# Optimization experiments

Measured on AMD Instinct MI355X. Metric: run time of the kernel, lower is better.

The kernel has to match this reference:

```python
import jax, jax.numpy as jnp
import numpy as np

NUM_CELLS, NUM_CLASSES = 25, 17
B = 65536
MULT = 16            # multiplier
OC = 64              # out_channels = out_features // 25
OUT_FEATURES = 1600
SLOPE = 0.01         # F.leaky_relu default negative_slope


def lrelu(x):
    return jax.nn.leaky_relu(x, SLOPE)


def setup_inputs() -> dict:
    key = jax.random.key(0)
    ks = jax.random.split(key, 9)
    s = 0.05
    return {
        "x": jax.random.randint(ks[0], (B, NUM_CELLS), 0, NUM_CLASSES, dtype=jnp.int64)
             if jax.config.jax_enable_x64 else
             jax.random.randint(ks[0], (B, NUM_CELLS), 0, NUM_CLASSES).astype(jnp.int32),
        # depthwise_full: Conv1d(17, 425, 25, groups=17) -> per-group [17, 25, 25]
        "W_df": jax.random.normal(ks[1], (NUM_CLASSES, NUM_CELLS, NUM_CELLS), jnp.float32) * s,
        "b_df": jnp.zeros((NUM_CLASSES * NUM_CELLS,), jnp.float32),
        # pointwise_full: Conv1d(425, 320, 1)
        "W_pf": jax.random.normal(ks[2], (OC * 5, NUM_CLASSES * NUM_CELLS), jnp.float32) * s,
        "b_pf": jax.random.normal(ks[3], (OC * 5,), jnp.float32) * s,
        # depthwise_hori: Conv2d(17, 272, (1,5), groups=17) -> [17, 16, 5]
        "W_dh": jax.random.normal(ks[4], (NUM_CLASSES, MULT, 5), jnp.float32) * s,
        "b_dh": jnp.zeros((NUM_CLASSES * MULT,), jnp.float32),
        "W_ph": jax.random.normal(ks[5], (OC, NUM_CLASSES * MULT), jnp.float32) * s,
        "b_ph": jax.random.normal(ks[5], (OC,), jnp.float32) * s,
        # depthwise_vert: Conv2d(17, 272, (5,1), groups=17) -> [17, 16, 5]
        "W_dv": jax.random.normal(ks[6], (NUM_CLASSES, MULT, 5), jnp.float32) * s,
        "b_dv": jnp.zeros((NUM_CLASSES * MULT,), jnp.float32),
        "W_pv": jax.random.normal(ks[7], (OC, NUM_CLASSES * MULT), jnp.float32) * s,
        "b_pv": jax.random.normal(ks[7], (OC,), jnp.float32) * s,
        # conv_out: Conv1d(64, 1600, 15)
        "W_out": jax.random.normal(ks[8], (OUT_FEATURES, OC, 15), jnp.float32) * s,
        "b_out": jnp.zeros((OUT_FEATURES,), jnp.float32),
    }


def reference(x, W_df, b_df, W_pf, b_pf, W_dh, b_dh, W_ph, b_ph,
              W_dv, b_dv, W_pv, b_pv, W_out, b_out):
    b = x.shape[0]
    oh = jax.nn.one_hot(x, NUM_CLASSES, dtype=jnp.float32)       # [B,25,17]
    xc = jnp.transpose(oh, (0, 2, 1))                            # [B,17,25]

    # full branch: depthwise conv1d k=25 over length-25 -> length 1
    full = jnp.einsum('bcl,cml->bcm', xc, W_df).reshape(b, -1) + b_df   # [B,425]
    full = lrelu(full)
    full = lrelu(full @ W_pf.T + b_pf)                           # [B,320]

    board = xc.reshape(b, NUM_CLASSES, 5, 5)                     # [B,17,5,5]

    # horizontal: depthwise (1,5) conv -> [B,272,5] (over rows)
    hori = jnp.einsum('bcrj,cmj->bcmr', board, W_dh).reshape(b, -1, 5) + b_dh[None, :, None]
    hori = lrelu(hori)
    hori = lrelu(jnp.einsum('bkr,ok->bor', hori, W_ph) + b_ph[None, :, None])  # [B,64,5]

    # vertical: depthwise (5,1) conv -> [B,272,5] (over cols)
    vert = jnp.einsum('bcrj,cmr->bcmj', board, W_dv).reshape(b, -1, 5) + b_dv[None, :, None]
    vert = lrelu(vert)
    vert = lrelu(jnp.einsum('bkj,ok->boj', vert, W_pv) + b_pv[None, :, None])  # [B,64,5]

    cat = jnp.concatenate([full.reshape(b, OC, 5), hori, vert], axis=2)        # [B,64,15]
    out = lrelu(jnp.einsum('bcl,ocl->bo', cat, W_out) + b_out)                 # [B,1600]
    return out
```

## Files before the change

### kernel.cpp

```cpp
#include <hip/hip_runtime.h>


typedef __bf16 bf16;
typedef bf16  bf16x8 __attribute__((ext_vector_type(8)));
typedef float f32x4  __attribute__((ext_vector_type(4)));

__device__ __forceinline__ float lrelu(float v) { return v > 0.f ? v : 0.01f * v; }

__device__ __forceinline__ void gl2lds16(const void* g, void* l) {
  __builtin_amdgcn_global_load_lds(
      (__attribute__((address_space(1))) void*)const_cast<void*>(g),
      (__attribute__((address_space(3))) void*)l, 16, 0, 0);
}

__device__ __forceinline__ void xcd_remap(int& mt, int& nt) {
  const int nxt    = gridDim.x;
  const int nwg    = gridDim.x * gridDim.y;
  const int linear = blockIdx.y * gridDim.x + blockIdx.x;
  const int xcd = linear & 7, pos = linear >> 3;
  const int q = nwg >> 3, r = nwg & 7;
  const int logical = (xcd < r ? xcd * (q + 1) : r * (q + 1) + (xcd - r) * q) + pos;
  mt = logical / nxt;
  nt = logical - mt * nxt;
}

__device__ void compute_U(float* __restrict__ U,
                          const float* __restrict__ Wd, const float* __restrict__ bd,
                          const float* __restrict__ Wp, const float* __restrict__ bp,
                          int c, int mask, int o) {
  float val;
  if (mask == 0) {
    if (c == 0) {
      float s = bp[o];
      for (int cc = 0; cc < 17; cc++)
        for (int m = 0; m < 16; m++)
          s += Wp[o * 272 + cc * 16 + m] * lrelu(bd[cc * 16 + m]);
      val = s;
    } else {
      val = 0.f;
    }
  } else {
    float s = 0.f;
    #pragma unroll
    for (int m = 0; m < 16; m++) {
      float z = bd[c * 16 + m];
      #pragma unroll
      for (int j = 0; j < 5; j++)
        if ((mask >> j) & 1) z += Wd[c * 80 + m * 5 + j];
      s += Wp[o * 272 + c * 16 + m] * (lrelu(z) - lrelu(bd[c * 16 + m]));
    }
    val = s;
  }
  U[(c * 32 + mask) * 64 + o] = val;
}

__global__ __launch_bounds__(256) void prep_kernel(
    const float* __restrict__ W_pf,
    const float* __restrict__ W_dh, const float* __restrict__ b_dh,
    const float* __restrict__ W_ph, const float* __restrict__ b_ph,
    const float* __restrict__ W_dv, const float* __restrict__ b_dv,
    const float* __restrict__ W_pv, const float* __restrict__ b_pv,
    const float* __restrict__ W_out,
    bf16* __restrict__ WbOT, bf16* __restrict__ WbPF,
    float* __restrict__ Uh, float* __restrict__ Uv) {
  int id = blockIdx.x * 256 + threadIdx.x;

  if (id < 1664 * 960) {
    int n = id / 960, k = id % 960;
    float v = 0.f;
    if (n < 1600) {
      int src;
      if (k < 320)      src = n * 960 + (k / 5) * 15 + (k % 5);
      else if (k < 640) { int kk = k - 320; src = n * 960 + (kk & 63) * 15 + 5  + (kk >> 6); }
      else              { int kk = k - 640; src = n * 960 + (kk & 63) * 15 + 10 + (kk >> 6); }
      v = W_out[src];
    }
    WbOT[id] = (bf16)v;
    return;
  }
  id -= 1664 * 960;

  if (id < 384 * 448) {
    int n = id / 448, k = id % 448;
    float v = (n < 320 && k < 425) ? W_pf[n * 425 + k] : 0.f;
    WbPF[id] = (bf16)v;
    return;
  }
  id -= 384 * 448;

  if (id < 17 * 32 * 64) {
    int o = id & 63, rest = id >> 6;
    compute_U(Uh, W_dh, b_dh, W_ph, b_ph, rest >> 5, rest & 31, o);
    return;
  }
  id -= 17 * 32 * 64;

  if (id < 17 * 32 * 64) {
    int o = id & 63, rest = id >> 6;
    compute_U(Uv, W_dv, b_dv, W_pv, b_pv, rest >> 5, rest & 31, o);
  }
}

#define AF_PAD 456

__global__ __launch_bounds__(256) void build_afull(
    const int* __restrict__ x, const float* __restrict__ W_df,
    const float* __restrict__ b_df, bf16* __restrict__ a_full) {
  __shared__ int  xs[64 * 25];
  __shared__ bf16 as[64 * AF_PAD];
  const int b0 = blockIdx.x * 64;
  for (int i = threadIdx.x; i < 64 * 25; i += 256) xs[i] = x[(long)b0 * 25 + i];
  __syncthreads();

  const int wave = threadIdx.x >> 6, lane = threadIdx.x & 63;
  for (int role = wave; role < 18; role += 4) {
    if (role < 17) {
      const int c = role;
      float acc[25];
      #pragma unroll
      for (int m = 0; m < 25; m++) acc[m] = 0.f;
      #pragma unroll
      for (int l = 0; l < 25; l++) {
        int xl = xs[lane * 25 + l];
        if (xl == c) {
          #pragma unroll
          for (int m = 0; m < 25; m++) acc[m] += W_df[c * 625 + m * 25 + l];
        }
      }
      #pragma unroll
      for (int m = 0; m < 25; m++)
        as[lane * AF_PAD + c * 25 + m] = (bf16)lrelu(acc[m] + b_df[c * 25 + m]);
    } else {
      for (int k = 425; k < 448; k++) as[lane * AF_PAD + k] = (bf16)0.f;
    }
  }
  __syncthreads();

  int4* dst = (int4*)(a_full + (long)b0 * 448);
  for (int i = threadIdx.x; i < 3584; i += 256) {
    int row = i / 56, off = i % 56;
    dst[i] = *(const int4*)((const char*)as + row * (AF_PAD * 2) + off * 16);
  }
}

__device__ __forceinline__ float group5(const float* __restrict__ U, int lane,
                                        int c0, int c1, int c2, int c3, int c4) {
  float acc = U[lane];
  {
    int m = 1 | ((int)(c1 == c0) << 1) | ((int)(c2 == c0) << 2) |
                ((int)(c3 == c0) << 3) | ((int)(c4 == c0) << 4);
    acc += U[(c0 * 32 + m) * 64 + lane];
  }
  if (c1 != c0) {
    int m = 2 | ((int)(c2 == c1) << 2) | ((int)(c3 == c1) << 3) | ((int)(c4 == c1) << 4);
    acc += U[(c1 * 32 + m) * 64 + lane];
  }
  if (c2 != c0 && c2 != c1) {
    int m = 4 | ((int)(c3 == c2) << 3) | ((int)(c4 == c2) << 4);
    acc += U[(c2 * 32 + m) * 64 + lane];
  }
  if (c3 != c0 && c3 != c1 && c3 != c2) {
    int m = 8 | ((int)(c4 == c3) << 4);
    acc += U[(c3 * 32 + m) * 64 + lane];
  }
  if (c4 != c0 && c4 != c1 && c4 != c2 && c4 != c3) {
    acc += U[(c4 * 32 + 16) * 64 + lane];
  }
  return lrelu(acc);
}

__global__ __launch_bounds__(256) void hv_kernel(
    const int* __restrict__ x, const float* __restrict__ Uh,
    const float* __restrict__ Uv, bf16* __restrict__ cat) {
  const int wave = threadIdx.x >> 6, lane = threadIdx.x & 63;
  const long b = (long)blockIdx.x * 4 + wave;
  const int* xb = x + b * 25;
  int xv[25];
  #pragma unroll
  for (int i = 0; i < 25; i++) xv[i] = xb[i];
  bf16* catb = cat + b * 960;
  #pragma unroll
  for (int r = 0; r < 5; r++) {
    float v = group5(Uh, lane, xv[5*r], xv[5*r+1], xv[5*r+2], xv[5*r+3], xv[5*r+4]);
    catb[320 + r * 64 + lane] = (bf16)v;
  }
  #pragma unroll
  for (int j = 0; j < 5; j++) {
    float v = group5(Uv, lane, xv[j], xv[5+j], xv[10+j], xv[15+j], xv[20+j]);
    catb[640 + j * 64 + lane] = (bf16)v;
  }
}

template <int KT, int MODE>
__global__ __launch_bounds__(256, 2) void gemm_bt(
    const bf16* __restrict__ A, const bf16* __restrict__ Bt,
    const float* __restrict__ bias, bf16* __restrict__ outb,
    float* __restrict__ outf, const int Nwrite, const int ldOut) {
  static_assert(KT % 32 == 0, "KT must be multiple of 32");
  __shared__ bf16 As[128 * 32];
  __shared__ bf16 Bs[128 * 32];

  const int tid = threadIdx.x;
  const int wave = tid >> 6, lane = tid & 63;
  int mt, nt;
  xcd_remap(mt, nt);

  const int  lrow = lane >> 2, lcol = lane & 3;
  const bf16* ag0 = A  + ((long)mt * 128 + wave * 32 + lrow) * KT + lcol * 8;
  const bf16* bg0 = Bt + ((long)nt * 128 + wave * 32 + lrow) * KT + lcol * 8;
  bf16* al = &As[(wave * 32 + lrow) * 32 + lcol * 8];
  bf16* bl = &Bs[(wave * 32 + lrow) * 32 + lcol * 8];

  const int wm = (wave & 1) * 64;
  const int wn = (wave >> 1) * 64;
  const int fr = lane & 15;
  const int fq = lane >> 4;

  f32x4 acc[4][4];
  #pragma unroll
  for (int i = 0; i < 4; i++)
    #pragma unroll
    for (int j = 0; j < 4; j++) acc[i][j] = f32x4{0.f, 0.f, 0.f, 0.f};

  for (int kt = 0; kt < KT / 32; kt++) {
    const int ko = kt * 32;
    gl2lds16(ag0 + ko, al);
    gl2lds16(ag0 + ko + (long)16 * KT, al + 16 * 32);
    gl2lds16(bg0 + ko, bl);
    gl2lds16(bg0 + ko + (long)16 * KT, bl + 16 * 32);
    __syncthreads();

    bf16x8 af[4], bfv[4];
    #pragma unroll
    for (int i = 0; i < 4; i++)
      af[i] = *(const bf16x8*)&As[(wm + i * 16 + fr) * 32 + fq * 8];
    #pragma unroll
    for (int j = 0; j < 4; j++)
      bfv[j] = *(const bf16x8*)&Bs[(wn + j * 16 + fr) * 32 + fq * 8];
    #pragma unroll
    for (int i = 0; i < 4; i++)
      #pragma unroll
      for (int j = 0; j < 4; j++)
        acc[i][j] = __builtin_amdgcn_mfma_f32_16x16x32_bf16(af[i], bfv[j], acc[i][j], 0, 0, 0);
    __syncthreads();
  }

  #pragma unroll
  for (int j = 0; j < 4; j++) {
    const int n = nt * 128 + wn + j * 16 + fr;
    const bool ok = n < Nwrite;
    const float bv = ok ? bias[n] : 0.f;
    #pragma unroll
    for (int i = 0; i < 4; i++) {
      const long row0 = (long)mt * 128 + wm + i * 16 + fq * 4;
      #pragma unroll
      for (int r = 0; r < 4; r++) {
        float v = lrelu(acc[i][j][r] + bv);
        if (ok) {
          if (MODE == 0) outb[(row0 + r) * (long)ldOut + n] = (bf16)v;
          else           outf[(row0 + r) * (long)ldOut + n] = v;
        }
      }
    }
  }
}

extern "C" void kernel_launch(void* const* d_in, const int* in_sizes, int n_in,
                              void* d_out, int out_size, void* d_ws, size_t ws_size,
                              hipStream_t stream) {
  const int*   x     = (const int*)d_in[0];
  const float* W_df  = (const float*)d_in[1];
  const float* b_df  = (const float*)d_in[2];
  const float* W_pf  = (const float*)d_in[3];
  const float* b_pf  = (const float*)d_in[4];
  const float* W_dh  = (const float*)d_in[5];
  const float* b_dh  = (const float*)d_in[6];
  const float* W_ph  = (const float*)d_in[7];
  const float* b_ph  = (const float*)d_in[8];
  const float* W_dv  = (const float*)d_in[9];
  const float* b_dv  = (const float*)d_in[10];
  const float* W_pv  = (const float*)d_in[11];
  const float* b_pv  = (const float*)d_in[12];
  const float* W_out = (const float*)d_in[13];
  const float* b_out = (const float*)d_in[14];
  float* out = (float*)d_out;

  const int B = in_sizes[0] / 25;

  char* ws = (char*)d_ws;
  size_t off = 0;
  bf16* cat   = (bf16*)(ws + off); off += (size_t)B * 960 * 2;
  bf16* afull = (bf16*)(ws + off); off += (size_t)B * 448 * 2;
  bf16* WbOT  = (bf16*)(ws + off); off += (size_t)1664 * 960 * 2;
  bf16* WbPF  = (bf16*)(ws + off); off += (size_t)384 * 448 * 2;
  float* Uh   = (float*)(ws + off); off += (size_t)17 * 32 * 64 * 4;
  float* Uv   = (float*)(ws + off); off += (size_t)17 * 32 * 64 * 4;

  const int prep_threads = 1664 * 960 + 384 * 448 + 2 * 17 * 32 * 64;
  prep_kernel<<<(prep_threads + 255) / 256, 256, 0, stream>>>(
      W_pf, W_dh, b_dh, W_ph, b_ph, W_dv, b_dv, W_pv, b_pv, W_out,
      WbOT, WbPF, Uh, Uv);

  build_afull<<<B / 64, 256, 0, stream>>>(x, W_df, b_df, afull);

  gemm_bt<448, 0><<<dim3(3, B / 128), 256, 0, stream>>>(
      afull, WbPF, b_pf, cat, nullptr, 320, 960);

  hv_kernel<<<B / 4, 256, 0, stream>>>(x, Uh, Uv, cat);

  gemm_bt<960, 1><<<dim3(13, B / 128), 256, 0, stream>>>(
      cat, WbOT, b_out, nullptr, out, 1600, 1600);
}
```

Baseline: 949.0 us.

## Triple-buffer LDS tiles in bf16 GEMM to overlap global loads with MFMA

Replaces the single-buffer load/sync/compute loop in gemm_bt with a 3-stage ring of LDS buffers. Loads for tile k+2 are issued before computing tile k, and explicit vmcnt waits plus one barrier per iteration replace the two __syncthreads. This is meant to hide global-to-LDS latency behind the matrix work. LDS use triples to 48KB per block, which may limit occupancy at two blocks per CU. It also depends on the vmcnt counts and the barrier ordering being correct.

```diff
diff --git a/kernel.cpp b/kernel.cpp
--- a/kernel.cpp
+++ b/kernel.cpp
@@ -197,8 +197,10 @@
     const float* __restrict__ bias, bf16* __restrict__ outb,
     float* __restrict__ outf, const int Nwrite, const int ldOut) {
   static_assert(KT % 32 == 0, "KT must be multiple of 32");
-  __shared__ bf16 As[128 * 32];
-  __shared__ bf16 Bs[128 * 32];
+  constexpr int NT = KT / 32;
+  static_assert(NT >= 3, "pipeline assumes at least 3 K-tiles");
+  __shared__ bf16 As[3][128 * 32];
+  __shared__ bf16 Bs[3][128 * 32];
 
   const int tid = threadIdx.x;
   const int wave = tid >> 6, lane = tid & 63;
@@ -208,8 +210,7 @@
   const int  lrow = lane >> 2, lcol = lane & 3;
   const bf16* ag0 = A  + ((long)mt * 128 + wave * 32 + lrow) * KT + lcol * 8;
   const bf16* bg0 = Bt + ((long)nt * 128 + wave * 32 + lrow) * KT + lcol * 8;
-  bf16* al = &As[(wave * 32 + lrow) * 32 + lcol * 8];
-  bf16* bl = &Bs[(wave * 32 + lrow) * 32 + lcol * 8];
+  const int lds_off = (wave * 32 + lrow) * 32 + lcol * 8;
 
   const int wm = (wave & 1) * 64;
   const int wn = (wave >> 1) * 64;
@@ -222,27 +223,55 @@
     #pragma unroll
     for (int j = 0; j < 4; j++) acc[i][j] = f32x4{0.f, 0.f, 0.f, 0.f};
 
-  for (int kt = 0; kt < KT / 32; kt++) {
-    const int ko = kt * 32;
-    gl2lds16(ag0 + ko, al);
-    gl2lds16(ag0 + ko + (long)16 * KT, al + 16 * 32);
-    gl2lds16(bg0 + ko, bl);
-    gl2lds16(bg0 + ko + (long)16 * KT, bl + 16 * 32);
-    __syncthreads();
-
+  {
+    gl2lds16(ag0 + 0,                 &As[0][lds_off]);
+    gl2lds16(ag0 + 0 + (long)16 * KT, &As[0][lds_off + 16 * 32]);
+    gl2lds16(bg0 + 0,                 &Bs[0][lds_off]);
+    gl2lds16(bg0 + 0 + (long)16 * KT, &Bs[0][lds_off + 16 * 32]);
+    gl2lds16(ag0 + 32,                 &As[1][lds_off]);
+    gl2lds16(ag0 + 32 + (long)16 * KT, &As[1][lds_off + 16 * 32]);
+    gl2lds16(bg0 + 32,                 &Bs[1][lds_off]);
+    gl2lds16(bg0 + 32 + (long)16 * KT, &Bs[1][lds_off + 16 * 32]);
+  }
+  asm volatile("s_waitcnt vmcnt(4)" ::: "memory");
+  __builtin_amdgcn_s_barrier();
+  asm volatile("" ::: "memory");
+
+  for (int kt = 0; kt < NT; kt++) {
+    const int cur = kt % 3;
+    if (kt + 2 < NT) {
+      const int nxt2 = (kt + 2) % 3;
+      const int ko = (kt + 2) * 32;
+      gl2lds16(ag0 + ko,                 &As[nxt2][lds_off]);
+      gl2lds16(ag0 + ko + (long)16 * KT, &As[nxt2][lds_off + 16 * 32]);
+      gl2lds16(bg0 + ko,                 &Bs[nxt2][lds_off]);
+      gl2lds16(bg0 + ko + (long)16 * KT, &Bs[nxt2][lds_off + 16 * 32]);
+    }
+
+    const bf16* Asb = As[cur];
+    const bf16* Bsb = Bs[cur];
     bf16x8 af[4], bfv[4];
     #pragma unroll
     for (int i = 0; i < 4; i++)
-      af[i] = *(const bf16x8*)&As[(wm + i * 16 + fr) * 32 + fq * 8];
+      af[i] = *(const bf16x8*)&Asb[(wm + i * 16 + fr) * 32 + fq * 8];
     #pragma unroll
     for (int j = 0; j < 4; j++)
-      bfv[j] = *(const bf16x8*)&Bs[(wn + j * 16 + fr) * 32 + fq * 8];
+      bfv[j] = *(const bf16x8*)&Bsb[(wn + j * 16 + fr) * 32 + fq * 8];
     #pragma unroll
     for (int i = 0; i < 4; i++)
       #pragma unroll
       for (int j = 0; j < 4; j++)
         acc[i][j] = __builtin_amdgcn_mfma_f32_16x16x32_bf16(af[i], bfv[j], acc[i][j], 0, 0, 0);
-    __syncthreads();
+
+    if (kt + 1 < NT) {
+      if (kt + 2 < NT) {
+        asm volatile("s_waitcnt vmcnt(4)" ::: "memory");
+      } else {
+        asm volatile("s_waitcnt vmcnt(0)" ::: "memory");
+      }
+      __builtin_amdgcn_s_barrier();
+      asm volatile("" ::: "memory");
+    }
   }
 
   #pragma unroll
```

Result: no change. 960.5 us (+1.2%).
